# Performance work log

Hardware: AMD Instinct MI355X
Metric: run time of the kernel (lower is better)

## Reference

```python
import jax, jax.numpy as jnp
import numpy as np

EMBED_DIM = 768
NUM_HEADS = 12


def setup_inputs() -> dict:
    key = jax.random.key(0)
    ks = jax.random.split(key, 9)
    B, N, C = 16, 1024, EMBED_DIM
    std = 1.0 / np.sqrt(C)
    x = jax.random.normal(ks[0], (B, N, C), dtype=jnp.float32)
    def w(k):
        return jax.random.normal(k, (C, C), dtype=jnp.float32) * std
    def b(k):
        return jax.random.normal(k, (C,), dtype=jnp.float32) * 0.01
    return {
        "x": x,
        "Wq": w(ks[1]), "bq": b(ks[2]),
        "Wk": w(ks[3]), "bk": b(ks[4]),
        "Wv": w(ks[5]), "bv": b(ks[6]),
        "Wo": w(ks[7]), "bo": b(ks[8]),
    }


def reference(x, Wq, bq, Wk, bk, Wv, bv, Wo, bo):
    B, N, C = x.shape
    H = NUM_HEADS
    Dh = C // H
    scale = 1.0 / np.sqrt(Dh)

    q = x @ Wq + bq  # (B, N, C)
    k = x @ Wk + bk
    v = x @ Wv + bv

    # Faithful to the original: (B, N, H, Dh) -> reshape(B*H, N, Dh)
    # WITHOUT transposing, exactly as torch_mla_core does (row-major reshape).
    q2 = q.reshape(B * H, N, Dh)
    k2 = k.reshape(B * H, N, Dh)
    v2 = v.reshape(B * H, N, Dh)

    scores = jnp.einsum('gld,gmd->glm', q2, k2) * scale  # (B*H, N, N)
    attn = jax.nn.softmax(scores, axis=-1)
    ctx2 = jnp.einsum('glm,gmd->gld', attn, v2)  # (B*H, N, Dh)

    ctx = ctx2.reshape(B, H, N, Dh).transpose(0, 2, 1, 3).reshape(B, N, C)
    out = ctx @ Wo + bo
    return out
```

## Files before the change

kernel.cpp:

```cpp
#include <hip/hip_runtime.h>
#include <hip/hip_bf16.h>
#include <cstdint>
#include <cstddef>

typedef unsigned short u16;
typedef __attribute__((ext_vector_type(8))) short s8v;
typedef __attribute__((ext_vector_type(4))) float f4v;
typedef __attribute__((ext_vector_type(8))) u16 u16x8;
typedef __attribute__((ext_vector_type(4))) uint32_t u32x4;

#define AS1 __attribute__((address_space(1)))
#define AS3 __attribute__((address_space(3)))

#define BATCH 16
#define SEQ   1024
#define EMBED 768
#define HEADS 12
#define DH    64
#define MTOT  (BATCH*SEQ)
#define QSCALE 0.1803368867f

__device__ __forceinline__ u16 f2bf(float f) {
    union { float f; uint32_t u; } v; v.f = f;
    uint32_t r = v.u + 0x7fffu + ((v.u >> 16) & 1u);
    return (u16)(r >> 16);
}

__device__ __forceinline__ float exp2_hw(float x) {
    float r;
    asm("v_exp_f32 %0, %1" : "=v"(r) : "v"(x));
    return r;
}

__device__ __forceinline__ void gll16(const u16* g, u16* l) {
    __builtin_amdgcn_global_load_lds((AS1 void*)g, (AS3 void*)l, 16, 0, 0);
}

#define XBLOCKS 12288
#define TBLOCKS 576
__global__ void k_pack(const float* __restrict__ x, u16* __restrict__ xb, int nx,
                       const float* __restrict__ Wq, const float* __restrict__ Wk,
                       const float* __restrict__ Wv, const float* __restrict__ Wo,
                       const float* __restrict__ bq, const float* __restrict__ bk,
                       const float* __restrict__ bv,
                       u16* __restrict__ wqkvT, u16* __restrict__ woT,
                       float* __restrict__ bqkv)
{
    __shared__ __attribute__((aligned(16))) u16 ts[64 * 80];
    const int tid = threadIdx.x;
    if (blockIdx.x < XBLOCKS) {
        int i = (blockIdx.x * 256 + tid) * 4;
        if (i + 3 < nx) {
            float4 f = *(const float4*)(x + i);
            ushort4 o;
            o.x = f2bf(f.x); o.y = f2bf(f.y); o.z = f2bf(f.z); o.w = f2bf(f.w);
            *(ushort4*)(xb + i) = o;
        }
        return;
    }
    int tb = blockIdx.x - XBLOCKS;
    if (tb < TBLOCKS) {
        const float* src; u16* dst; int n0, k0, nn0; float sc;
        if (tb < 432) {
            int nt = tb % 36, kt = tb / 36;
            n0 = nt * 64; k0 = kt * 64; dst = wqkvT;
            if (n0 < 768)       { src = Wq; nn0 = n0;        sc = QSCALE; }
            else if (n0 < 1536) { src = Wk; nn0 = n0 - 768;  sc = 1.0f;   }
            else                { src = Wv; nn0 = n0 - 1536; sc = 1.0f;   }
        } else {
            int tb2 = tb - 432;
            int nt = tb2 % 12, kt = tb2 / 12;
            n0 = nt * 64; k0 = kt * 64; nn0 = n0; sc = 1.0f;
            src = Wo; dst = woT;
        }
        const int r = tid >> 2, cb = (tid & 3) * 16;
#pragma unroll
        for (int i = 0; i < 4; ++i) {
            float4 f = *(const float4*)(src + (size_t)(k0 + r) * 768 + nn0 + cb + i * 4);
            ts[(cb + i * 4 + 0) * 80 + r] = f2bf(f.x * sc);
            ts[(cb + i * 4 + 1) * 80 + r] = f2bf(f.y * sc);
            ts[(cb + i * 4 + 2) * 80 + r] = f2bf(f.z * sc);
            ts[(cb + i * 4 + 3) * 80 + r] = f2bf(f.w * sc);
        }
        __syncthreads();
#pragma unroll
        for (int j = 0; j < 2; ++j) {
            u16x8 tv = *(const u16x8*)(ts + r * 80 + cb + j * 8);
            *(u16x8*)(dst + (size_t)(n0 + r) * 768 + k0 + cb + j * 8) = tv;
        }
        return;
    }
    int t3 = (tb - TBLOCKS) * 256 + tid;
    if (t3 < 2304) {
        bqkv[t3] = (t3 < 768) ? bq[t3] * QSCALE
                 : ((t3 < 1536) ? bk[t3 - 768] : bv[t3 - 1536]);
    }
}

template<int MODE>
__global__ __launch_bounds__(256) void k_gemm(
    const u16* __restrict__ A, const u16* __restrict__ BT,
    const float* __restrict__ bias,
    u16* __restrict__ oq, u16* __restrict__ okk, u16* __restrict__ ov,
    float* __restrict__ of)
{
    __shared__ __attribute__((aligned(16))) u16 As[2][128 * 64];
    __shared__ __attribute__((aligned(16))) u16 Bs[2][128 * 64];
    const int tid = threadIdx.x;
    const int m0 = blockIdx.x * 128;
    const int n0 = blockIdx.y * 128;
    const int wv = tid >> 6;
    const int ln = tid & 63;
    const int l15 = ln & 15, quad = ln >> 4;
    const int wm = (wv >> 1) * 64, wn = (wv & 1) * 64;

    const int srow = tid >> 3;
    const int schnk = ((tid & 7) ^ (srow & 7)) * 8;
    const u16* gA = A + (size_t)(m0 + srow) * 768 + schnk;
    const u16* gB = BT + (size_t)(n0 + srow) * 768 + schnk;
    const int lofs = wv * 512;

#define STG(buf, kt) { \
    const int ko_ = (kt) * 64; \
    _Pragma("unroll") \
    for (int i = 0; i < 4; ++i) { \
        gll16(gA + (size_t)i * 32 * 768 + ko_, &As[buf][0] + lofs + i * 2048); \
        gll16(gB + (size_t)i * 32 * 768 + ko_, &Bs[buf][0] + lofs + i * 2048); \
    } }

    const int sl0 = ((quad)     ^ (l15 & 7)) * 8;
    const int sl1 = ((4 + quad) ^ (l15 & 7)) * 8;

    f4v acc[4][4] = {};

    STG(0, 0);
    asm volatile("s_waitcnt vmcnt(0)" ::: "memory");
    __builtin_amdgcn_s_barrier();
    __builtin_amdgcn_sched_barrier(0);

    for (int kt = 0; kt < 12; ++kt) {
        const int cur = kt & 1;
        const u16* Ac = &As[cur][0];
        const u16* Bc = &Bs[cur][0];
        if (kt < 11) STG(cur ^ 1, kt + 1);

        s8v aF[4][2];
#pragma unroll
        for (int i = 0; i < 4; ++i) {
            const u16* base = Ac + (wm + i * 16 + l15) * 64;
            aF[i][0] = *(const s8v*)(base + sl0);
            aF[i][1] = *(const s8v*)(base + sl1);
        }
#pragma unroll
        for (int j = 0; j < 4; ++j) {
            const u16* base = Bc + (wn + j * 16 + l15) * 64;
            s8v bF0 = *(const s8v*)(base + sl0);
            s8v bF1 = *(const s8v*)(base + sl1);
#pragma unroll
            for (int i = 0; i < 4; ++i) {
                acc[i][j] = __builtin_amdgcn_mfma_f32_16x16x32_bf16(aF[i][0], bF0, acc[i][j], 0, 0, 0);
                acc[i][j] = __builtin_amdgcn_mfma_f32_16x16x32_bf16(aF[i][1], bF1, acc[i][j], 0, 0, 0);
            }
        }
        asm volatile("s_waitcnt vmcnt(0)" ::: "memory");
        __builtin_amdgcn_s_barrier();
        __builtin_amdgcn_sched_barrier(0);
    }
#undef STG

#pragma unroll
    for (int j = 0; j < 4; ++j) {
        int n = n0 + wn + j * 16 + l15;
        float bs = bias[n];
        if (MODE == 0) {
            u16* dst; int nn;
            if (n < 768)       { dst = oq;  nn = n; }
            else if (n < 1536) { dst = okk; nn = n - 768; }
            else               { dst = ov;  nn = n - 1536; }
#pragma unroll
            for (int i = 0; i < 4; ++i) {
                int mrow = m0 + wm + i * 16 + quad * 4;
#pragma unroll
                for (int rg = 0; rg < 4; ++rg)
                    dst[(size_t)(mrow + rg) * 768 + nn] = f2bf(acc[i][j][rg] + bs);
            }
        } else {
#pragma unroll
            for (int i = 0; i < 4; ++i) {
                int mrow = m0 + wm + i * 16 + quad * 4;
#pragma unroll
                for (int rg = 0; rg < 4; ++rg)
                    of[(size_t)(mrow + rg) * 768 + n] = acc[i][j][rg] + bs;
            }
        }
    }
}

__global__ void k_transpose_v(const u16* __restrict__ v, u16* __restrict__ vt) {
    __shared__ __attribute__((aligned(16))) u16 ts[64 * 80];
    int g = blockIdx.x >> 4;
    int l0 = (blockIdx.x & 15) << 6;
    const u16* vg = v + (size_t)g * 65536;
    u16* vtg = vt + (size_t)g * 65536;
    int tid = threadIdx.x;
#pragma unroll
    for (int c = tid; c < 512; c += 256) {
        int l = c >> 3, d0 = (c & 7) * 8;
        *(uint4*)(ts + l * 80 + d0) = *(const uint4*)(vg + (size_t)(l0 + l) * 64 + d0);
    }
    __syncthreads();
#pragma unroll
    for (int c = tid; c < 512; c += 256) {
        int d = c >> 3, lc = (c & 7) * 8;
        u16x8 tv;
#pragma unroll
        for (int i = 0; i < 8; ++i) tv[i] = ts[(lc + i) * 80 + d];
        *(u16x8*)(vtg + (size_t)d * 1024 + l0 + lc) = tv;
    }
}

#define KS2(r_, c_) ( ((r_) << 6) + (((((c_) >> 3) ^ ((r_) & 7)) & 7) << 3) + ((c_) & 7) )

__global__ __launch_bounds__(512) void k_attn(
    const u16* __restrict__ qb, const u16* __restrict__ kb,
    const u16* __restrict__ vt, u16* __restrict__ ctx)
{
    __shared__ __attribute__((aligned(16))) u16 Ks[128 * 64];
    __shared__ __attribute__((aligned(16))) u16 Vts[80 * 136];

    const int bid = blockIdx.x;
    const int xr = bid & 7, bt = bid >> 3;
    const int g = xr * 24 + (bt >> 2);
    const int q0 = (bt & 3) << 8;
    const int tid = threadIdx.x, wv = tid >> 6;
    const int ln = tid & 63, l15 = ln & 15, quad = ln >> 4;
    const u16* qg = qb + (size_t)g * 65536;
    const u16* kg = kb + (size_t)g * 65536;
    const u16* vtg = vt + (size_t)g * 65536;

    const int krr = tid >> 3, kcb = (tid & 7) * 8;
    const int vd = tid >> 4, vc0 = (tid & 15) * 8;
    const u16* kgp = kg + (size_t)krr * 64 + kcb;
    const u16* vgp = vtg + (size_t)vd * 1024 + vc0;

    uint4 kr0 = *(const uint4*)(kgp);
    uint4 kr1 = *(const uint4*)(kgp + 4096);
    uint4 vr0 = *(const uint4*)(vgp);
    uint4 vr1 = *(const uint4*)(vgp + 32768);

    if (tid < 16) {
        uint4 ones;
        ones.x = 0x3F803F80u; ones.y = 0x3F803F80u;
        ones.z = 0x3F803F80u; ones.w = 0x3F803F80u;
        *(uint4*)(Vts + 64 * 136 + tid * 8) = ones;
    }

    const u16* qrow = qg + (size_t)(q0 + wv * 32 + l15) * 64 + quad * 8;
    s8v aQ00 = *(const s8v*)qrow;
    s8v aQ01 = *(const s8v*)(qrow + 32);
    s8v aQ10 = *(const s8v*)(qrow + 1024);
    s8v aQ11 = *(const s8v*)(qrow + 1024 + 32);

    f4v o0[4] = {}, o1[4] = {};
    f4v o4_0 = {}, o4_1 = {};

    for (int jt = 0; jt < 8; ++jt) {
        __builtin_amdgcn_s_barrier();
        __builtin_amdgcn_sched_barrier(0);

        *(uint4*)(Ks + KS2(krr,      kcb)) = kr0;
        *(uint4*)(Ks + KS2(krr + 64, kcb)) = kr1;
        *(uint4*)(Vts + (vd     ) * 136 + vc0) = vr0;
        *(uint4*)(Vts + (vd + 32) * 136 + vc0) = vr1;

        if (jt < 7) {
            const size_t koff = (size_t)(jt + 1) * 8192;
            const int voff = (jt + 1) * 128;
            kr0 = *(const uint4*)(kgp + koff);
            kr1 = *(const uint4*)(kgp + koff + 4096);
            vr0 = *(const uint4*)(vgp + voff);
            vr1 = *(const uint4*)(vgp + voff + 32768);
        }

        asm volatile("s_waitcnt lgkmcnt(0)" ::: "memory");
        __builtin_amdgcn_s_barrier();
        __builtin_amdgcn_sched_barrier(0);

        f4v s0[8], s1[8];
        __builtin_amdgcn_s_setprio(1);
#pragma unroll
        for (int ns = 0; ns < 8; ++ns) {
            int rK = ns * 16 + l15;
            s8v b0 = *(const s8v*)(Ks + KS2(rK, quad * 8));
            s8v b1 = *(const s8v*)(Ks + KS2(rK, quad * 8 + 32));
            f4v t0 = {};
            t0 = __builtin_amdgcn_mfma_f32_16x16x32_bf16(b0, aQ00, t0, 0, 0, 0);
            t0 = __builtin_amdgcn_mfma_f32_16x16x32_bf16(b1, aQ01, t0, 0, 0, 0);
            s0[ns] = t0;
            f4v t1 = {};
            t1 = __builtin_amdgcn_mfma_f32_16x16x32_bf16(b0, aQ10, t1, 0, 0, 0);
            t1 = __builtin_amdgcn_mfma_f32_16x16x32_bf16(b1, aQ11, t1, 0, 0, 0);
            s1[ns] = t1;
        }
        __builtin_amdgcn_s_setprio(0);

        s8v aP0[4], aP1[4];
#pragma unroll
        for (int ns = 0; ns < 8; ++ns)
#pragma unroll
            for (int rg = 0; rg < 4; ++rg)
                s0[ns][rg] = exp2_hw(s0[ns][rg]);
#pragma unroll
        for (int ks = 0; ks < 4; ++ks) {
            uint32_t a0, a1, c0, c1;
            asm("v_cvt_pk_bf16_f32 %0, %1, %2" : "=v"(a0) : "v"(s0[2*ks][0]),   "v"(s0[2*ks][1]));
            asm("v_cvt_pk_bf16_f32 %0, %1, %2" : "=v"(a1) : "v"(s0[2*ks][2]),   "v"(s0[2*ks][3]));
            asm("v_cvt_pk_bf16_f32 %0, %1, %2" : "=v"(c0) : "v"(s0[2*ks+1][0]), "v"(s0[2*ks+1][1]));
            asm("v_cvt_pk_bf16_f32 %0, %1, %2" : "=v"(c1) : "v"(s0[2*ks+1][2]), "v"(s0[2*ks+1][3]));
            asm("v_permlane32_swap_b32 %0, %1" : "+v"(a0), "+v"(c0));
            asm("v_permlane16_swap_b32 %0, %1" : "+v"(a0), "+v"(c0));
            asm("v_permlane32_swap_b32 %0, %1" : "+v"(a1), "+v"(c1));
            asm("v_permlane16_swap_b32 %0, %1" : "+v"(a1), "+v"(c1));
            u32x4 pk; pk.x = a0; pk.y = a1; pk.z = c0; pk.w = c1;
            aP0[ks] = __builtin_bit_cast(s8v, pk);
        }
#pragma unroll
        for (int ns = 0; ns < 8; ++ns)
#pragma unroll
            for (int rg = 0; rg < 4; ++rg)
                s1[ns][rg] = exp2_hw(s1[ns][rg]);
#pragma unroll
        for (int ks = 0; ks < 4; ++ks) {
            uint32_t a0, a1, c0, c1;
            asm("v_cvt_pk_bf16_f32 %0, %1, %2" : "=v"(a0) : "v"(s1[2*ks][0]),   "v"(s1[2*ks][1]));
            asm("v_cvt_pk_bf16_f32 %0, %1, %2" : "=v"(a1) : "v"(s1[2*ks][2]),   "v"(s1[2*ks][3]));
            asm("v_cvt_pk_bf16_f32 %0, %1, %2" : "=v"(c0) : "v"(s1[2*ks+1][0]), "v"(s1[2*ks+1][1]));
            asm("v_cvt_pk_bf16_f32 %0, %1, %2" : "=v"(c1) : "v"(s1[2*ks+1][2]), "v"(s1[2*ks+1][3]));
            asm("v_permlane32_swap_b32 %0, %1" : "+v"(a0), "+v"(c0));
            asm("v_permlane16_swap_b32 %0, %1" : "+v"(a0), "+v"(c0));
            asm("v_permlane32_swap_b32 %0, %1" : "+v"(a1), "+v"(c1));
            asm("v_permlane16_swap_b32 %0, %1" : "+v"(a1), "+v"(c1));
            u32x4 pk; pk.x = a0; pk.y = a1; pk.z = c0; pk.w = c1;
            aP1[ks] = __builtin_bit_cast(s8v, pk);
        }

        __builtin_amdgcn_s_setprio(1);
#pragma unroll
        for (int ks = 0; ks < 4; ++ks) {
#pragma unroll
            for (int ds = 0; ds < 4; ++ds) {
                s8v bV = *(const s8v*)(Vts + (ds * 16 + l15) * 136 + ks * 32 + quad * 8);
                o0[ds] = __builtin_amdgcn_mfma_f32_16x16x32_bf16(aP0[ks], bV, o0[ds], 0, 0, 0);
                o1[ds] = __builtin_amdgcn_mfma_f32_16x16x32_bf16(aP1[ks], bV, o1[ds], 0, 0, 0);
            }
            s8v bV4 = *(const s8v*)(Vts + (64 + l15) * 136 + ks * 32 + quad * 8);
            o4_0 = __builtin_amdgcn_mfma_f32_16x16x32_bf16(aP0[ks], bV4, o4_0, 0, 0, 0);
            o4_1 = __builtin_amdgcn_mfma_f32_16x16x32_bf16(aP1[ks], bV4, o4_1, 0, 0, 0);
        }
        __builtin_amdgcn_s_setprio(0);
    }

    const int b = g / 12, h = g % 12;
    u16* cbase = ctx + (size_t)b * 786432 + h * 64;
#pragma unroll
    for (int rg = 0; rg < 4; ++rg) {
        int row0 = q0 + wv * 32 + quad * 4 + rg;
        float inv0 = 1.0f / __shfl(o4_0[rg], quad << 4, 64);
#pragma unroll
        for (int ds = 0; ds < 4; ++ds)
            cbase[(size_t)row0 * 768 + ds * 16 + l15] = f2bf(o0[ds][rg] * inv0);
        int row1 = row0 + 16;
        float inv1 = 1.0f / __shfl(o4_1[rg], quad << 4, 64);
#pragma unroll
        for (int ds = 0; ds < 4; ++ds)
            cbase[(size_t)row1 * 768 + ds * 16 + l15] = f2bf(o1[ds][rg] * inv1);
    }
}

extern "C" void kernel_launch(void* const* d_in, const int* in_sizes, int n_in,
                              void* d_out, int out_size, void* d_ws, size_t ws_size,
                              hipStream_t stream) {
    const float* x  = (const float*)d_in[0];
    const float* Wq = (const float*)d_in[1];
    const float* bq = (const float*)d_in[2];
    const float* Wk = (const float*)d_in[3];
    const float* bk = (const float*)d_in[4];
    const float* Wv = (const float*)d_in[5];
    const float* bv = (const float*)d_in[6];
    const float* Wo = (const float*)d_in[7];
    const float* bo = (const float*)d_in[8];
    float* out = (float*)d_out;

    const size_t NTOK = (size_t)MTOT * EMBED;
    char* w = (char*)d_ws;
    u16* xb    = (u16*)w;              w += NTOK * 2;
    u16* qb    = (u16*)w;              w += NTOK * 2;
    u16* kb    = (u16*)w;              w += NTOK * 2;
    u16* vb    = (u16*)w;              w += NTOK * 2;
    u16* vtb   = (u16*)w;              w += NTOK * 2;
    u16* wqkvT = (u16*)w;              w += (size_t)2304 * 768 * 2;
    u16* woT   = (u16*)w;              w += (size_t)768 * 768 * 2;
    float* bqkv = (float*)w;           w += 2304 * 4;
    u16* ctx = xb;

    k_pack<<<XBLOCKS + TBLOCKS + 9, 256, 0, stream>>>(x, xb, (int)NTOK,
        Wq, Wk, Wv, Wo, bq, bk, bv, wqkvT, woT, bqkv);

    dim3 g1(128, 18);
    k_gemm<0><<<g1, 256, 0, stream>>>(xb, wqkvT, bqkv, qb, kb, vb, nullptr);

    k_transpose_v<<<3072, 256, 0, stream>>>(vb, vtb);
    k_attn<<<768, 512, 0, stream>>>(qb, kb, vtb, ctx);

    dim3 g2(128, 6);
    k_gemm<1><<<g2, 256, 0, stream>>>(ctx, woT, bo, nullptr, nullptr, nullptr, out);
}
```

Baseline: 312.6 us.

## Triple-buffer GEMM LDS with BK=32 and two-stage-ahead prefetch

Changes the bf16 GEMM mainloop from double-buffered 64-wide K tiles to triple-buffered 32-wide K tiles, issuing global-to-LDS loads two iterations ahead. The vmcnt wait is relaxed to vmcnt(4), so the loads for the next tile stay in flight while the current one is consumed. The aim is to hide global load latency better and cut the stall at each barrier. In exchange there are twice as many barriers and iterations, less MFMA work per barrier, and a narrower XOR swizzle that may raise LDS bank conflicts.

```diff
diff --git a/kernel.cpp b/kernel.cpp
--- a/kernel.cpp
+++ b/kernel.cpp
@@ -104,8 +104,8 @@
     u16* __restrict__ oq, u16* __restrict__ okk, u16* __restrict__ ov,
     float* __restrict__ of)
 {
-    __shared__ __attribute__((aligned(16))) u16 As[2][128 * 64];
-    __shared__ __attribute__((aligned(16))) u16 Bs[2][128 * 64];
+    __shared__ __attribute__((aligned(16))) u16 As[3][128 * 32];
+    __shared__ __attribute__((aligned(16))) u16 Bs[3][128 * 32];
     const int tid = threadIdx.x;
     const int m0 = blockIdx.x * 128;
     const int n0 = blockIdx.y * 128;
@@ -114,57 +114,56 @@
     const int l15 = ln & 15, quad = ln >> 4;
     const int wm = (wv >> 1) * 64, wn = (wv & 1) * 64;
 
-    const int srow = tid >> 3;
-    const int schnk = ((tid & 7) ^ (srow & 7)) * 8;
+    const int srow = tid >> 2;
+    const int schnk = ((tid & 3) ^ (srow & 3)) * 8;
     const u16* gA = A + (size_t)(m0 + srow) * 768 + schnk;
     const u16* gB = BT + (size_t)(n0 + srow) * 768 + schnk;
     const int lofs = wv * 512;
 
 #define STG(buf, kt) { \
-    const int ko_ = (kt) * 64; \
-    _Pragma("unroll") \
-    for (int i = 0; i < 4; ++i) { \
-        gll16(gA + (size_t)i * 32 * 768 + ko_, &As[buf][0] + lofs + i * 2048); \
-        gll16(gB + (size_t)i * 32 * 768 + ko_, &Bs[buf][0] + lofs + i * 2048); \
-    } }
-
-    const int sl0 = ((quad)     ^ (l15 & 7)) * 8;
-    const int sl1 = ((4 + quad) ^ (l15 & 7)) * 8;
+    const int ko_ = (kt) * 32; \
+    gll16(gA + ko_,         As[buf] + lofs); \
+    gll16(gA + 49152 + ko_, As[buf] + lofs + 2048); \
+    gll16(gB + ko_,         Bs[buf] + lofs); \
+    gll16(gB + 49152 + ko_, Bs[buf] + lofs + 2048); }
+
+    const int slc = ((quad ^ (l15 & 3)) * 8);
 
     f4v acc[4][4] = {};
 
     STG(0, 0);
-    asm volatile("s_waitcnt vmcnt(0)" ::: "memory");
+    STG(1, 1);
+    asm volatile("s_waitcnt vmcnt(4)" ::: "memory");
     __builtin_amdgcn_s_barrier();
     __builtin_amdgcn_sched_barrier(0);
 
-    for (int kt = 0; kt < 12; ++kt) {
-        const int cur = kt & 1;
-        const u16* Ac = &As[cur][0];
-        const u16* Bc = &Bs[cur][0];
-        if (kt < 11) STG(cur ^ 1, kt + 1);
-
-        s8v aF[4][2];
-#pragma unroll
-        for (int i = 0; i < 4; ++i) {
-            const u16* base = Ac + (wm + i * 16 + l15) * 64;
-            aF[i][0] = *(const s8v*)(base + sl0);
-            aF[i][1] = *(const s8v*)(base + sl1);
-        }
-#pragma unroll
-        for (int j = 0; j < 4; ++j) {
-            const u16* base = Bc + (wn + j * 16 + l15) * 64;
-            s8v bF0 = *(const s8v*)(base + sl0);
-            s8v bF1 = *(const s8v*)(base + sl1);
-#pragma unroll
-            for (int i = 0; i < 4; ++i) {
-                acc[i][j] = __builtin_amdgcn_mfma_f32_16x16x32_bf16(aF[i][0], bF0, acc[i][j], 0, 0, 0);
-                acc[i][j] = __builtin_amdgcn_mfma_f32_16x16x32_bf16(aF[i][1], bF1, acc[i][j], 0, 0, 0);
-            }
-        }
-        asm volatile("s_waitcnt vmcnt(0)" ::: "memory");
+    int cb = 0;
+#pragma unroll 3
+    for (int kt = 0; kt < 24; ++kt) {
+        int sb = cb + 2; if (sb >= 3) sb -= 3;
+        if (kt < 22) STG(sb, kt + 2);
+
+        const u16* Ac = As[cb];
+        const u16* Bc = Bs[cb];
+        s8v aF[4], bF[4];
+#pragma unroll
+        for (int i = 0; i < 4; ++i)
+            aF[i] = *(const s8v*)(Ac + (wm + i * 16 + l15) * 32 + slc);
+#pragma unroll
+        for (int j = 0; j < 4; ++j)
+            bF[j] = *(const s8v*)(Bc + (wn + j * 16 + l15) * 32 + slc);
+#pragma unroll
+        for (int i = 0; i < 4; ++i)
+#pragma unroll
+            for (int j = 0; j < 4; ++j)
+                acc[i][j] = __builtin_amdgcn_mfma_f32_16x16x32_bf16(aF[i], bF[j], acc[i][j], 0, 0, 0);
+
+        if (kt < 22) { asm volatile("s_waitcnt vmcnt(4)" ::: "memory"); }
+        else         { asm volatile("s_waitcnt vmcnt(0)" ::: "memory"); }
         __builtin_amdgcn_s_barrier();
         __builtin_amdgcn_sched_barrier(0);
+
+        cb = (cb == 2) ? 0 : cb + 1;
     }
 #undef STG
 
```

Result: slower. 334.0 us (+6.9%).
